# Kernel optimization log

Measured on AMD Instinct MI355X. Metric: run time of the kernel, lower is better.

Reference implementation:

```python
import jax, jax.numpy as jnp
import numpy as np

B, N, K, D = 8, 4096, 16, 256


def layer_norm(x, g, b, eps=1e-5):
    m = jnp.mean(x, axis=-1, keepdims=True)
    v = jnp.var(x, axis=-1, keepdims=True)
    return (x - m) * jax.lax.rsqrt(v + eps) * g + b


def setup_inputs() -> dict:
    key = jax.random.key(0)
    ks = jax.random.split(key, 8)

    def lin(k, fi, fo):
        return (jax.random.normal(k, (fi, fo), jnp.float32) / np.sqrt(fi).astype(np.float32),
                jnp.zeros((fo,), jnp.float32))

    coordinates = jax.random.normal(ks[0], (B, N, 3), jnp.float32)
    W1, b1 = lin(ks[1], 10, D // 4)
    W2, b2 = lin(ks[2], D // 4, D // 2)
    W3, b3 = lin(ks[3], D // 2, D)
    Wa1, ba1 = lin(ks[4], D, D)
    Wa2, ba2 = lin(ks[5], D, D)
    return {
        'coordinates': coordinates,
        'W1': W1, 'b1': b1, 'g1': jnp.ones((D // 4,)), 'be1': jnp.zeros((D // 4,)),
        'W2': W2, 'b2': b2, 'g2': jnp.ones((D // 2,)), 'be2': jnp.zeros((D // 2,)),
        'W3': W3, 'b3': b3, 'g3': jnp.ones((D,)), 'be3': jnp.zeros((D,)),
        'Wa1': Wa1, 'ba1': ba1, 'ga1': jnp.ones((D,)), 'bea1': jnp.zeros((D,)),
        'Wa2': Wa2, 'ba2': ba2,
    }


def reference(coordinates, W1, b1, g1, be1, W2, b2, g2, be2, W3, b3, g3, be3,
              Wa1, ba1, ga1, bea1, Wa2, ba2):
    # kNN via squared-distance matrix (monotone in Euclidean distance)
    sq = jnp.sum(coordinates * coordinates, axis=-1)  # [B,N]
    d2 = sq[:, :, None] + sq[:, None, :] - 2.0 * jnp.einsum('bnd,bmd->bnm', coordinates, coordinates)
    _, idx = jax.lax.top_k(-d2, K)  # smallest K distances, [B,N,K]

    nbr = jax.vmap(lambda c, i: c[i])(coordinates, idx)  # [B,N,K,3]
    rel = nbr - coordinates[:, :, None, :]               # relative positions
    dist = jnp.linalg.norm(rel, axis=-1, keepdims=True)  # [B,N,K,1]
    rn = rel / (dist + 1e-6)
    axy = jnp.arctan2(rn[..., 1], rn[..., 0])[..., None]
    axz = jnp.arctan2(rn[..., 2], rn[..., 0])[..., None]
    ayz = jnp.arctan2(rn[..., 2], rn[..., 1])[..., None]
    geom = jnp.concatenate([dist, rel, axy, axz, ayz, rn], axis=-1)  # [B,N,K,10]

    # encoder MLP
    h = jax.nn.relu(layer_norm(geom @ W1 + b1, g1, be1))
    h = jax.nn.relu(layer_norm(h @ W2 + b2, g2, be2))
    h = layer_norm(h @ W3 + b3, g3, be3)

    agg = jnp.mean(h, axis=2)  # mean over neighbors -> [B,N,D]

    # aggregator MLP
    out = jax.nn.relu(layer_norm(agg @ Wa1 + ba1, ga1, bea1)) @ Wa2 + ba2
    return out
```

## Files before the change

### kernel.cpp

```cpp
#include <hip/hip_runtime.h>
#include <hip/hip_bf16.h>
#include <math.h>

#define BB 8
#define NN 4096
#define KK 16
#define DD 256

typedef __hip_bfloat16 bf16;
typedef _Float16 half8 __attribute__((ext_vector_type(8)));
typedef float f32x4 __attribute__((ext_vector_type(4)));

union HFU { _Float16 h; unsigned short u; };
__device__ __forceinline__ unsigned short f2h(float x) { HFU v; v.h = (_Float16)x; return v.u; }

#define CONV_TOTAL 273344
#define O_COORD 0
#define O_W1 98304
#define O_b1 98944
#define O_g1 99008
#define O_be1 99072
#define O_W2 99136
#define O_b2 107328
#define O_g2 107456
#define O_be2 107584
#define O_W3 107712
#define O_b3 140480
#define O_g3 140736
#define O_be3 140992
#define O_Wa1 141248
#define O_ba1 206784
#define O_ga1 207040
#define O_bea1 207296
#define O_Wa2 207552
#define O_ba2 273088

#define F_W1 0
#define F_W2 2048
#define F_W3 10240
#define F_A1 43008
#define F_A2 108544
#define FRAG_TOTAL 174080

struct SrcPtrs {
  const void* p[19];
};

__global__ __launch_bounds__(256) void convert_kernel(SrcPtrs sp, float* __restrict__ dst) {
  static constexpr int OFF[20] = {
      0,      98304,  98944,  99008,  99072,  99136,  107328, 107456, 107584,
      107712, 140480, 140736, 140992, 141248, 206784, 207040, 207296, 207552,
      273088, 273344};
  const int i = blockIdx.x * 256 + threadIdx.x;
  if (i >= CONV_TOTAL) return;
  const unsigned tag = ((const unsigned*)sp.p[3])[0];
  const bool isb = (tag == 0x3F803F80u);
  int s = 0;
#pragma unroll
  for (int j = 1; j < 19; j++)
    if (i >= OFF[j]) s = j;
  const int local = i - OFF[s];
  float v = isb ? __bfloat162float(((const bf16*)sp.p[s])[local])
                : ((const float*)sp.p[s])[local];
  dst[i] = v;
}

__global__ __launch_bounds__(256) void swizzle_kernel(const float* __restrict__ conv,
                                                      unsigned short* __restrict__ frag) {
  const int t = blockIdx.x * 256 + threadIdx.x;
  if (t >= FRAG_TOTAL) return;
  int l, e;
  if (t < 2048) { l = 0; e = t; }
  else if (t < 10240) { l = 1; e = t - 2048; }
  else if (t < 43008) { l = 2; e = t - 10240; }
  else if (t < 108544) { l = 3; e = t - 43008; }
  else { l = 4; e = t - 108544; }
  static constexpr int WOFF[5] = {O_W1, O_W2, O_W3, O_Wa1, O_Wa2};
  static constexpr int NDIM[5] = {64, 128, 256, 256, 256};
  static constexpr int NTC[5] = {4, 8, 16, 16, 16};
  static constexpr int KREAL[5] = {10, 64, 128, 256, 256};
  static constexpr int HOFF[5] = {F_W1, F_W2, F_W3, F_A1, F_A2};
  const int j = e & 7;
  const int lane = (e >> 3) & 63;
  const int tile = e >> 9;
  const int nt = tile % NTC[l];
  const int kt = tile / NTC[l];
  const int k = kt * 32 + (lane >> 4) * 8 + j;
  const int n = nt * 16 + (lane & 15);
  float w = (k < KREAL[l]) ? conv[WOFF[l] + k * NDIM[l] + n] : 0.0f;
  frag[HOFF[l] + e] = f2h(w);
}

__device__ __forceinline__ float sq3_rn(float x, float y, float z) {
  return __fadd_rn(__fadd_rn(__fmul_rn(x, x), __fmul_rn(y, y)), __fmul_rn(z, z));
}
__device__ __forceinline__ float dot3_rn(float ax, float ay, float az, float bx, float by, float bz) {
  return __fadd_rn(__fadd_rn(__fmul_rn(ax, bx), __fmul_rn(ay, by)), __fmul_rn(az, bz));
}
__device__ __forceinline__ unsigned f2ord(float f) {
  unsigned u = __float_as_uint(f);
  return (u & 0x80000000u) ? ~u : (u | 0x80000000u);
}
__device__ __forceinline__ float ord2f(unsigned o) {
  unsigned u = (o & 0x80000000u) ? (o & 0x7FFFFFFFu) : ~o;
  return __uint_as_float(u);
}

__device__ __forceinline__ unsigned long long bitonic64(unsigned long long key, int lane) {
#pragma unroll
  for (int k = 2; k <= 64; k <<= 1) {
#pragma unroll
    for (int jj = k >> 1; jj > 0; jj >>= 1) {
      unsigned long long v = __shfl_xor(key, jj, 64);
      bool asc = ((lane & k) == 0);
      bool up = ((lane & jj) != 0);
      unsigned long long mn = (key < v) ? key : v;
      unsigned long long mx2 = (key < v) ? v : key;
      key = (up == asc) ? mx2 : mn;
    }
  }
  return key;
}

__global__ __launch_bounds__(256) void prep_kernel(const float* __restrict__ conv,
                                                   float4* __restrict__ soa) {
  const int i = blockIdx.x * 256 + threadIdx.x;
  if (i >= BB * NN) return;
  const float* c = conv + O_COORD + (size_t)i * 3;
  float x = c[0], y = c[1], z = c[2];
  soa[i] = make_float4(x, y, z, sq3_rn(x, y, z));
}

__global__ __launch_bounds__(256) void knn_wave_kernel(const float4* __restrict__ soa,
                                                       int* __restrict__ idx_out) {
  const int lane = threadIdx.x & 63;
  const int wid = (blockIdx.x * 256 + threadIdx.x) >> 6;
  const int q0 = wid * 4;
  const int b = q0 >> 12;
  const float4* P = soa + (size_t)b * NN;

  float cx[4], cy[4], cz[4], sqn[4];
#pragma unroll
  for (int j = 0; j < 4; j++) {
    float4 c = P[(q0 + j) & (NN - 1)];
    cx[j] = c.x; cy[j] = c.y; cz[j] = c.z; sqn[j] = c.w;
  }

  unsigned long long R[4], pend[4];
  float tauf[4];
  int A[4] = {0, 0, 0, 0};
#pragma unroll
  for (int j = 0; j < 4; j++) pend[j] = ~0ull;

  float4 c0 = P[lane];
  float4 cnext = P[64 + lane];

  auto MERGE = [&](int j) {
    unsigned long long key =
        (lane < 16) ? R[j] : ((lane < 16 + A[j]) ? pend[j] : ~0ull);
    key = bitonic64(key, lane);
    R[j] = key;
    tauf[j] = ord2f((unsigned)(unsigned long long)__builtin_amdgcn_readlane(
        (int)(unsigned)(key >> 32), 15));
    A[j] = 0;
  };

  auto APPEND = [&](int j, unsigned long long msk, int cc, unsigned long long key) {
    unsigned rank = __builtin_amdgcn_mbcnt_hi(
        (unsigned)(msk >> 32), __builtin_amdgcn_mbcnt_lo((unsigned)msk, 0u));
    const bool flag = ((msk >> lane) & 1ull) != 0;
    const int dst = flag ? (16 + A[j] + (int)rank) : (lane & 15);
    int src = __builtin_amdgcn_ds_permute(dst << 2, lane) & 63;
    unsigned lo = (unsigned)__builtin_amdgcn_ds_bpermute(src << 2, (int)(unsigned)key);
    unsigned hi = (unsigned)__builtin_amdgcn_ds_bpermute(src << 2, (int)(unsigned)(key >> 32));
    const bool cons = (lane >= 16 + A[j]) && (lane < 16 + A[j] + cc);
    if (cons) pend[j] = (((unsigned long long)hi) << 32) | lo;
    A[j] += cc;
  };

#pragma unroll
  for (int j = 0; j < 4; j++) {
    float dot = dot3_rn(cx[j], cy[j], cz[j], c0.x, c0.y, c0.z);
    float d2 = __fsub_rn(__fadd_rn(sqn[j], c0.w), __fmul_rn(2.0f, dot));
    unsigned long long key = (((unsigned long long)f2ord(d2)) << 32) | (unsigned)lane;
    key = bitonic64(key, lane);
    R[j] = key;
    tauf[j] = ord2f((unsigned)(unsigned long long)__builtin_amdgcn_readlane(
        (int)(unsigned)(key >> 32), 15));
  }

  for (int bt = 1; bt < 64; bt++) {
    const float4 c = cnext;
    if (bt < 63) cnext = P[(bt + 1) * 64 + lane];
    const int m0 = bt * 64;
    float d2v[4];
    unsigned long long pm[4];
#pragma unroll
    for (int j = 0; j < 4; j++) {
      float dot = dot3_rn(cx[j], cy[j], cz[j], c.x, c.y, c.z);
      d2v[j] = __fsub_rn(__fadd_rn(sqn[j], c.w), __fmul_rn(2.0f, dot));
      pm[j] = __ballot(d2v[j] <= tauf[j]);
    }
    if (!(pm[0] | pm[1] | pm[2] | pm[3])) continue;
#pragma unroll
    for (int j = 0; j < 4; j++) {
      unsigned long long rem = pm[j];
      if (!rem) continue;
      const unsigned long long key =
          (((unsigned long long)f2ord(d2v[j])) << 32) | (unsigned)(m0 + lane);
      int cc = __builtin_popcountll(rem);
      while (A[j] + cc > 48) {
        if (A[j] == 0) {
          unsigned long long take = rem & 0xFFFFFFFFull;
          APPEND(j, take, __builtin_popcountll(take), key);
          rem ^= take;
        }
        MERGE(j);
        rem &= __ballot(d2v[j] <= tauf[j]);
        cc = __builtin_popcountll(rem);
      }
      APPEND(j, rem, cc, key);
    }
  }

#pragma unroll
  for (int j = 0; j < 4; j++) {
    if (A[j]) MERGE(j);
    if (lane < KK)
      idx_out[(size_t)(q0 + j) * KK + lane] = (int)(R[j] & 0xFFFFFFFFull);
  }
}

template <int KT>
__device__ __forceinline__ void load_afrags(half8* A, const unsigned short* lF,
                                            int rowe, int lane) {
#pragma unroll
  for (int kt = 0; kt < KT; kt++) {
    int off = (lane & 15) * rowe + kt * 32 + (lane >> 4) * 8;
    A[kt] = *reinterpret_cast<const half8*>(lF + off);
  }
}

template <int NT>
__device__ __forceinline__ void init_acc(f32x4* acc, const float* __restrict__ bias,
                                         int lane) {
  const int col = lane & 15;
#pragma unroll
  for (int nt = 0; nt < NT; nt++) {
    float bv = bias[nt * 16 + col];
    acc[nt] = {bv, bv, bv, bv};
  }
}

template <int KT, int NT>
__device__ __forceinline__ void gemm_acc(f32x4* acc, const half8* A,
                                         const unsigned short* bb, int lane) {
#pragma unroll
  for (int kt = 0; kt < KT; kt++)
#pragma unroll
    for (int nt = 0; nt < NT; nt++) {
      const half8 bf = *reinterpret_cast<const half8*>(bb + (kt * NT + nt) * 512 + lane * 8);
      acc[nt] = __builtin_amdgcn_mfma_f32_16x16x32_f16(A[kt], bf, acc[nt], 0, 0, 0);
    }
}

template <int NT>
__device__ __forceinline__ void ln_stats(const f32x4* acc, float* m, float* rs) {
  float s[4] = {0.f, 0.f, 0.f, 0.f}, s2[4] = {0.f, 0.f, 0.f, 0.f};
#pragma unroll
  for (int nt = 0; nt < NT; nt++)
#pragma unroll
    for (int r = 0; r < 4; r++) {
      float v = acc[nt][r];
      s[r] += v;
      s2[r] += v * v;
    }
#pragma unroll
  for (int msk = 1; msk <= 8; msk <<= 1)
#pragma unroll
    for (int r = 0; r < 4; r++) {
      s[r] += __shfl_xor(s[r], msk, 64);
      s2[r] += __shfl_xor(s2[r], msk, 64);
    }
  const float invN = 1.0f / (NT * 16);
#pragma unroll
  for (int r = 0; r < 4; r++) {
    m[r] = s[r] * invN;
    float var = s2[r] * invN - m[r] * m[r];
    rs[r] = rsqrtf(var + 1e-5f);
  }
}

template <int NT, bool RELU>
__device__ __forceinline__ void ln_store(const f32x4* acc, const float* m, const float* rs,
                                         const float* __restrict__ g, const float* __restrict__ be,
                                         unsigned short* lF, int rowe, int lane) {
  const int col = lane & 15;
  const int rbase = (lane >> 4) * 4;
#pragma unroll
  for (int nt = 0; nt < NT; nt++) {
    float gv = g[nt * 16 + col], bv = be[nt * 16 + col];
#pragma unroll
    for (int r = 0; r < 4; r++) {
      float v = (acc[nt][r] - m[r]) * rs[r] * gv + bv;
      if (RELU) v = fmaxf(v, 0.0f);
      lF[(rbase + r) * rowe + nt * 16 + col] = f2h(v);
    }
  }
}

__device__ __forceinline__ void stage_b(unsigned short* bbuf,
                                        const unsigned short* __restrict__ src,
                                        int n_u4, int tid) {
  const uint4* s = reinterpret_cast<const uint4*>(src);
  uint4* d = reinterpret_cast<uint4*>(bbuf);
  for (int i = tid; i < n_u4; i += 256) d[i] = s[i];
}

#define ROWE_E 136
#define PSTR_E (16 * ROWE_E)

__global__ __launch_bounds__(256, 3) void encoder_mfma(
    const float* __restrict__ conv, const int* __restrict__ nbr,
    const unsigned short* __restrict__ frag, unsigned short* __restrict__ agF) {
  __shared__ unsigned short planes[4 * PSTR_E];
  __shared__ unsigned short Bbuf[16384];
  const int tid = threadIdx.x;
  const int lane = tid & 63;
  const int wave = tid >> 6;
  const int point = blockIdx.x * 4 + wave;
  const int b = point >> 12;
  const int n = point & (NN - 1);
  const float* cb = conv + O_COORD + (size_t)b * NN * 3;
  unsigned short* lF = planes + wave * PSTR_E;

  {
    int pl = tid >> 6, row = (tid >> 2) & 15, part = tid & 3;
    *reinterpret_cast<uint4*>(planes + pl * PSTR_E + row * ROWE_E + part * 8) =
        make_uint4(0u, 0u, 0u, 0u);
    stage_b(Bbuf, frag + F_W1, 1280, tid);
  }
  __syncthreads();

  if (lane < 16) {
    float cx = cb[n * 3 + 0], cy = cb[n * 3 + 1], cz = cb[n * 3 + 2];
    int id = nbr[(size_t)point * KK + lane];
    float rx = __fsub_rn(cb[id * 3 + 0], cx);
    float ry = __fsub_rn(cb[id * 3 + 1], cy);
    float rz = __fsub_rn(cb[id * 3 + 2], cz);
    float dist = __fsqrt_rn(sq3_rn(rx, ry, rz));
    float den = __fadd_rn(dist, 1e-6f);
    float ux = __fdiv_rn(rx, den), uy = __fdiv_rn(ry, den), uz = __fdiv_rn(rz, den);
    float ge[10];
    ge[0] = dist; ge[1] = rx; ge[2] = ry; ge[3] = rz;
    ge[4] = atan2f(uy, ux); ge[5] = atan2f(uz, ux); ge[6] = atan2f(uz, uy);
    ge[7] = ux; ge[8] = uy; ge[9] = uz;
#pragma unroll
    for (int c = 0; c < 10; c++) lF[lane * ROWE_E + c] = f2h(ge[c]);
  }

  float m[4], rs[4];
  {
    half8 A[1];
    load_afrags<1>(A, lF, ROWE_E, lane);
    f32x4 acc1[4];
    init_acc<4>(acc1, conv + O_b1, lane);
    gemm_acc<1, 4>(acc1, A, Bbuf, lane);
    ln_stats<4>(acc1, m, rs);
    ln_store<4, true>(acc1, m, rs, conv + O_g1, conv + O_be1, lF, ROWE_E, lane);
  }
  {
    half8 A[2];
    load_afrags<2>(A, lF, ROWE_E, lane);
    f32x4 acc2[8];
    init_acc<8>(acc2, conv + O_b2, lane);
    gemm_acc<2, 8>(acc2, A, Bbuf + 2048, lane);
    ln_stats<8>(acc2, m, rs);
    ln_store<8, true>(acc2, m, rs, conv + O_g2, conv + O_be2, lF, ROWE_E, lane);
  }
  half8 A3[4];
  load_afrags<4>(A3, lF, ROWE_E, lane);
  f32x4 acc[16];
  init_acc<16>(acc, conv + O_b3, lane);
  __syncthreads();
  stage_b(Bbuf, frag + F_W3, 2048, tid);
  __syncthreads();
  gemm_acc<2, 16>(acc, A3, Bbuf, lane);
  __syncthreads();
  stage_b(Bbuf, frag + F_W3 + 16384, 2048, tid);
  __syncthreads();
  gemm_acc<2, 16>(acc, A3 + 2, Bbuf, lane);

  {
    ln_stats<16>(acc, m, rs);
    const int col = lane & 15;
    float sv[16];
#pragma unroll
    for (int nt = 0; nt < 16; nt++) {
      float gv = conv[O_g3 + nt * 16 + col], bv = conv[O_be3 + nt * 16 + col];
      float s = 0.f;
#pragma unroll
      for (int r = 0; r < 4; r++) s += (acc[nt][r] - m[r]) * rs[r] * gv + bv;
      s += __shfl_xor(s, 16, 64);
      s += __shfl_xor(s, 32, 64);
      sv[nt] = s * (1.0f / 16.0f);
    }
    if (lane < 16) {
      size_t base = (size_t)point * DD;
#pragma unroll
      for (int nt = 0; nt < 16; nt++) agF[base + nt * 16 + lane] = f2h(sv[nt]);
    }
  }
}

#define ROWE_A 264

__global__ __launch_bounds__(256) void aggmlp_mfma(
    const float* __restrict__ conv, const unsigned short* __restrict__ agF,
    const unsigned short* __restrict__ a1, const unsigned short* __restrict__ a2,
    const unsigned* __restrict__ g1raw, void* __restrict__ out) {
  __shared__ unsigned short lds[4][16 * ROWE_A];
  const int lane = threadIdx.x & 63;
  const int wave = threadIdx.x >> 6;
  const int row0 = (blockIdx.x * 4 + wave) * 16;
  unsigned short* lF = lds[wave];

#pragma unroll
  for (int t = 0; t < 8; t++) {
    int v = t * 64 + lane;
    int row = v >> 5;
    int c0 = (v & 31) * 8;
    *reinterpret_cast<uint4*>(lF + row * ROWE_A + c0) =
        *reinterpret_cast<const uint4*>(agF + ((size_t)(row0 + row) * DD + c0));
  }
  __syncthreads();

  float m[4], rs[4];
  f32x4 acc[16];
  {
    half8 A[8];
    load_afrags<8>(A, lF, ROWE_A, lane);
    init_acc<16>(acc, conv + O_ba1, lane);
    gemm_acc<8, 16>(acc, A, a1, lane);
    ln_stats<16>(acc, m, rs);
    ln_store<16, true>(acc, m, rs, conv + O_ga1, conv + O_bea1, lF, ROWE_A, lane);
  }
  __syncthreads();
  {
    half8 A[8];
    load_afrags<8>(A, lF, ROWE_A, lane);
    init_acc<16>(acc, conv + O_ba2, lane);
    gemm_acc<8, 16>(acc, A, a2, lane);
  }
  const bool isb = (g1raw[0] == 0x3F803F80u);
  const int col = lane & 15;
  const int rbase = (lane >> 4) * 4;
  if (isb) {
    bf16* o = (bf16*)out;
#pragma unroll
    for (int nt = 0; nt < 16; nt++)
#pragma unroll
      for (int r = 0; r < 4; r++)
        o[(size_t)(row0 + rbase + r) * DD + nt * 16 + col] = __float2bfloat16(acc[nt][r]);
  } else {
    float* o = (float*)out;
#pragma unroll
    for (int nt = 0; nt < 16; nt++)
#pragma unroll
      for (int r = 0; r < 4; r++)
        o[(size_t)(row0 + rbase + r) * DD + nt * 16 + col] = acc[nt][r];
  }
}

extern "C" void kernel_launch(void* const* d_in, const int* in_sizes, int n_in,
                              void* d_out, int out_size, void* d_ws, size_t ws_size,
                              hipStream_t stream) {
  char* ws = (char*)d_ws;
  float* conv = (float*)ws;
  int* idx_ws = (int*)(ws + 1093376);
  unsigned short* agF = (unsigned short*)(ws + 3190528);
  unsigned short* frag = (unsigned short*)(ws + 19967744);
  float4* soa = (float4*)(ws + 20315904);

  SrcPtrs sp;
  for (int i = 0; i < 19; i++) sp.p[i] = d_in[i];

  convert_kernel<<<(CONV_TOTAL + 255) / 256, 256, 0, stream>>>(sp, conv);
  swizzle_kernel<<<(FRAG_TOTAL + 255) / 256, 256, 0, stream>>>(conv, frag);
  prep_kernel<<<(BB * NN + 255) / 256, 256, 0, stream>>>(conv, soa);

  knn_wave_kernel<<<BB * NN / 16, 256, 0, stream>>>(soa, idx_ws);

  encoder_mfma<<<BB * NN / 4, 256, 0, stream>>>(conv, idx_ws, frag, agF);

  aggmlp_mfma<<<BB * NN / 64, 256, 0, stream>>>(conv, agF, frag + F_A1, frag + F_A2,
                                                (const unsigned*)d_in[3], d_out);
}
```

Before: 419.6 us.

## Spatially sort points into Morton-ordered grid cells before brute-force kNN scan

Adds a per-batch counting-sort kernel that bins points into an 8x8x8 Morton-ordered grid and writes sorted coordinates plus original indices. The kNN kernel then processes spatially coherent query groups and scans candidate blocks starting near the query's own block, so the top-16 threshold tightens early and fewer candidates pass the ballot, reducing merge and append work. The scan still covers all points, so results stay exact, but ties could be broken differently because keys now carry original indices in a different visit order. The kNN kernel also moves to 64-thread blocks and changes how APPEND places non-flagged lanes.

```diff
diff --git a/kernel.cpp b/kernel.cpp
--- a/kernel.cpp
+++ b/kernel.cpp
@@ -122,28 +122,71 @@
   return key;
 }
 
-__global__ __launch_bounds__(256) void prep_kernel(const float* __restrict__ conv,
-                                                   float4* __restrict__ soa) {
-  const int i = blockIdx.x * 256 + threadIdx.x;
-  if (i >= BB * NN) return;
-  const float* c = conv + O_COORD + (size_t)i * 3;
-  float x = c[0], y = c[1], z = c[2];
-  soa[i] = make_float4(x, y, z, sq3_rn(x, y, z));
-}
-
-__global__ __launch_bounds__(256) void knn_wave_kernel(const float4* __restrict__ soa,
-                                                       int* __restrict__ idx_out) {
-  const int lane = threadIdx.x & 63;
-  const int wid = (blockIdx.x * 256 + threadIdx.x) >> 6;
+__global__ __launch_bounds__(512) void cellsort_kernel(const float* __restrict__ conv,
+                                                       float4* __restrict__ sorted,
+                                                       int* __restrict__ sidx) {
+  __shared__ unsigned hist[512];
+  __shared__ unsigned scanb[512];
+  const int b = blockIdx.x;
+  const int tid = threadIdx.x;
+  const float* cb = conv + O_COORD + (size_t)b * NN * 3;
+  hist[tid] = 0;
+  __syncthreads();
+  float xs[8], ys[8], zs[8];
+  int cell[8];
+  unsigned rank[8];
+#pragma unroll
+  for (int u = 0; u < 8; u++) {
+    int p = u * 512 + tid;
+    float x = cb[p * 3 + 0], y = cb[p * 3 + 1], z = cb[p * 3 + 2];
+    xs[u] = x; ys[u] = y; zs[u] = z;
+    int ix = min(7, max(0, (int)floorf(x + 4.0f)));
+    int iy = min(7, max(0, (int)floorf(y + 4.0f)));
+    int iz = min(7, max(0, (int)floorf(z + 4.0f)));
+    int m = ((ix & 1) | ((ix & 2) << 2) | ((ix & 4) << 4)) |
+            (((iy & 1) | ((iy & 2) << 2) | ((iy & 4) << 4)) << 1) |
+            (((iz & 1) | ((iz & 2) << 2) | ((iz & 4) << 4)) << 2);
+    cell[u] = m;
+    rank[u] = atomicAdd(&hist[m], 1u);
+  }
+  __syncthreads();
+  scanb[tid] = hist[tid];
+  __syncthreads();
+  for (int off = 1; off < 512; off <<= 1) {
+    unsigned t = (tid >= off) ? scanb[tid - off] : 0u;
+    __syncthreads();
+    scanb[tid] += t;
+    __syncthreads();
+  }
+#pragma unroll
+  for (int u = 0; u < 8; u++) {
+    unsigned base = scanb[cell[u]] - hist[cell[u]];
+    unsigned pos = base + rank[u];
+    sorted[(size_t)b * NN + pos] =
+        make_float4(xs[u], ys[u], zs[u], sq3_rn(xs[u], ys[u], zs[u]));
+    sidx[(size_t)b * NN + pos] = u * 512 + tid;
+  }
+}
+
+__global__ __launch_bounds__(64) void knn_wave_kernel(const float4* __restrict__ soa,
+                                                      const int* __restrict__ sI,
+                                                      int* __restrict__ idx_out) {
+  const int lane = threadIdx.x;
+  const int wid = blockIdx.x;
   const int q0 = wid * 4;
   const int b = q0 >> 12;
   const float4* P = soa + (size_t)b * NN;
+  const int* I = sI + (size_t)b * NN;
+  const int qr = q0 & (NN - 1);
+  const int base = qr >> 6;
 
   float cx[4], cy[4], cz[4], sqn[4];
+  int qix[4];
 #pragma unroll
   for (int j = 0; j < 4; j++) {
-    float4 c = P[(q0 + j) & (NN - 1)];
+    float4 c = P[qr + j];
     cx[j] = c.x; cy[j] = c.y; cz[j] = c.z; sqn[j] = c.w;
+    qix[j] = I[qr + j];
   }
 
   unsigned long long R[4], pend[4];
@@ -151,9 +194,6 @@
   int A[4] = {0, 0, 0, 0};
 #pragma unroll
   for (int j = 0; j < 4; j++) pend[j] = ~0ull;
-
-  float4 c0 = P[lane];
-  float4 cnext = P[64 + lane];
 
   auto MERGE = [&](int j) {
     unsigned long long key =
@@ -169,30 +209,48 @@
     unsigned rank = __builtin_amdgcn_mbcnt_hi(
         (unsigned)(msk >> 32), __builtin_amdgcn_mbcnt_lo((unsigned)msk, 0u));
     const bool flag = ((msk >> lane) & 1ull) != 0;
-    const int dst = flag ? (16 + A[j] + (int)rank) : (lane & 15);
+    const int lim = 16 + A[j];
+    const int nf = lane - (int)rank;
+    const int dst = flag ? (lim + (int)rank) : (nf < lim ? nf : nf + cc);
     int src = __builtin_amdgcn_ds_permute(dst << 2, lane) & 63;
     unsigned lo = (unsigned)__builtin_amdgcn_ds_bpermute(src << 2, (int)(unsigned)key);
     unsigned hi = (unsigned)__builtin_amdgcn_ds_bpermute(src << 2, (int)(unsigned)(key >> 32));
-    const bool cons = (lane >= 16 + A[j]) && (lane < 16 + A[j] + cc);
+    const bool cons = (lane >= lim) && (lane < lim + cc);
     if (cons) pend[j] = (((unsigned long long)hi) << 32) | lo;
     A[j] += cc;
   };
 
+  const int b0 = base * 64 + lane;
+  float4 f0 = P[b0];
+  int i0 = I[b0];
+  const int b1 = ((base + 1) & 63) * 64 + lane;
+  float4 f1 = P[b1];
+  int i1 = I[b1];
+  const int b2i = ((base + 2) & 63) * 64 + lane;
+  float4 f2 = P[b2i];
+  int i2 = I[b2i];
+
 #pragma unroll
   for (int j = 0; j < 4; j++) {
-    float dot = dot3_rn(cx[j], cy[j], cz[j], c0.x, c0.y, c0.z);
-    float d2 = __fsub_rn(__fadd_rn(sqn[j], c0.w), __fmul_rn(2.0f, dot));
-    unsigned long long key = (((unsigned long long)f2ord(d2)) << 32) | (unsigned)lane;
+    float dot = dot3_rn(cx[j], cy[j], cz[j], f0.x, f0.y, f0.z);
+    float d2 = __fsub_rn(__fadd_rn(sqn[j], f0.w), __fmul_rn(2.0f, dot));
+    unsigned long long key =
+        (((unsigned long long)f2ord(d2)) << 32) | (unsigned)i0;
     key = bitonic64(key, lane);
     R[j] = key;
     tauf[j] = ord2f((unsigned)(unsigned long long)__builtin_amdgcn_readlane(
         (int)(unsigned)(key >> 32), 15));
   }
 
-  for (int bt = 1; bt < 64; bt++) {
-    const float4 c = cnext;
-    if (bt < 63) cnext = P[(bt + 1) * 64 + lane];
-    const int m0 = bt * 64;
+  for (int t = 1; t < 64; t++) {
+    const float4 c = f1;
+    const int iv = i1;
+    f1 = f2; i1 = i2;
+    if (t + 2 < 64) {
+      const int nb = ((base + t + 2) & 63) * 64 + lane;
+      f2 = P[nb];
+      i2 = I[nb];
+    }
     float d2v[4];
     unsigned long long pm[4];
 #pragma unroll
@@ -207,7 +265,7 @@
       unsigned long long rem = pm[j];
       if (!rem) continue;
       const unsigned long long key =
-          (((unsigned long long)f2ord(d2v[j])) << 32) | (unsigned)(m0 + lane);
+          (((unsigned long long)f2ord(d2v[j])) << 32) | (unsigned)iv;
       int cc = __builtin_popcountll(rem);
       while (A[j] + cc > 48) {
         if (A[j] == 0) {
@@ -219,7 +277,7 @@
         rem &= __ballot(d2v[j] <= tauf[j]);
         cc = __builtin_popcountll(rem);
       }
-      APPEND(j, rem, cc, key);
+      if (cc) APPEND(j, rem, cc, key);
     }
   }
 
@@ -227,7 +285,8 @@
   for (int j = 0; j < 4; j++) {
     if (A[j]) MERGE(j);
     if (lane < KK)
-      idx_out[(size_t)(q0 + j) * KK + lane] = (int)(R[j] & 0xFFFFFFFFull);
+      idx_out[((size_t)b * NN + (unsigned)qix[j]) * KK + lane] =
+          (int)(R[j] & 0xFFFFFFFFull);
   }
 }
 
@@ -480,16 +539,17 @@
   int* idx_ws = (int*)(ws + 1093376);
   unsigned short* agF = (unsigned short*)(ws + 3190528);
   unsigned short* frag = (unsigned short*)(ws + 19967744);
-  float4* soa = (float4*)(ws + 20315904);
+  float4* sorted = (float4*)(ws + 20315904);
+  int* sidx = (int*)(ws + 20840192);
 
   SrcPtrs sp;
   for (int i = 0; i < 19; i++) sp.p[i] = d_in[i];
 
   convert_kernel<<<(CONV_TOTAL + 255) / 256, 256, 0, stream>>>(sp, conv);
   swizzle_kernel<<<(FRAG_TOTAL + 255) / 256, 256, 0, stream>>>(conv, frag);
-  prep_kernel<<<(BB * NN + 255) / 256, 256, 0, stream>>>(conv, soa);
-
-  knn_wave_kernel<<<BB * NN / 16, 256, 0, stream>>>(soa, idx_ws);
+  cellsort_kernel<<<BB, 512, 0, stream>>>(conv, sorted, sidx);
+
+  knn_wave_kernel<<<BB * NN / 4, 64, 0, stream>>>(sorted, sidx, idx_ws);
 
   encoder_mfma<<<BB * NN / 4, 256, 0, stream>>>(conv, idx_ws, frag, agF);
 
```

Measured after the change: 391.3 us. -6.8%, faster.
